# Kernel tuning notes

Hardware: AMD Instinct MI355X
Metric: run time of the kernel (lower is better)

## Reference

```python
import jax, jax.numpy as jnp
import numpy as np

V, E, H, L = 512, 128, 256, 4
B, T = 128, 1024


def setup_inputs() -> dict:
    key = jax.random.key(0)
    ks = jax.random.split(key, 16)
    s = 0.05
    inp = {
        "x": jax.random.randint(ks[0], (B, T), 0, V),
        "tags": jax.random.randint(ks[1], (B, T), 0, L),
        "mask": jnp.ones((B, T), dtype=bool),
        "emb": jax.random.normal(ks[2], (V, E), jnp.float32) * s,
        "w_ih_f": jax.random.normal(ks[3], (3 * H, E), jnp.float32) * s,
        "w_hh_f": jax.random.normal(ks[4], (3 * H, H), jnp.float32) * s,
        "b_ih_f": jax.random.normal(ks[5], (3 * H,), jnp.float32) * s,
        "b_hh_f": jax.random.normal(ks[6], (3 * H,), jnp.float32) * s,
        "w_ih_b": jax.random.normal(ks[7], (3 * H, E), jnp.float32) * s,
        "w_hh_b": jax.random.normal(ks[8], (3 * H, H), jnp.float32) * s,
        "b_ih_b": jax.random.normal(ks[9], (3 * H,), jnp.float32) * s,
        "b_hh_b": jax.random.normal(ks[10], (3 * H,), jnp.float32) * s,
        "fc_w": jax.random.normal(ks[11], (L, 2 * H), jnp.float32) * s,
        "fc_b": jax.random.normal(ks[12], (L,), jnp.float32) * s,
        "start_trans": jax.random.normal(ks[13], (L,), jnp.float32) * 0.1,
        "end_trans": jax.random.normal(ks[14], (L,), jnp.float32) * 0.1,
        "trans": jax.random.normal(ks[15], (L, L), jnp.float32) * 0.1,
    }
    return inp


def _gru_scan(xe, w_ih, w_hh, b_ih, b_hh):
    # xe: [B,T,E] -> out [B,T,H]; PyTorch GRU gate order: r, z, n
    gi = jnp.einsum("bte,ge->btg", xe, w_ih) + b_ih  # [B,T,3H]
    gi = jnp.swapaxes(gi, 0, 1)  # [T,B,3H]
    h0 = jnp.zeros((xe.shape[0], H), xe.dtype)

    def step(h, gi_t):
        gh = h @ w_hh.T + b_hh
        i_r, i_z, i_n = jnp.split(gi_t, 3, axis=-1)
        h_r, h_z, h_n = jnp.split(gh, 3, axis=-1)
        r = jax.nn.sigmoid(i_r + h_r)
        z = jax.nn.sigmoid(i_z + h_z)
        n = jnp.tanh(i_n + r * h_n)
        h_new = (1.0 - z) * n + z * h
        return h_new, h_new

    _, out = jax.lax.scan(step, h0, gi)
    return jnp.swapaxes(out, 0, 1)  # [B,T,H]


def _crf_neg_llh(emissions, tags, mask, start_trans, end_trans, trans):
    # emissions [B,T,L], tags [B,T] int, mask [B,T] bool
    maskf = mask.astype(emissions.dtype)
    # ----- numerator: score of gold path -----
    em_sel = jnp.take_along_axis(emissions, tags[..., None], axis=2)[..., 0]  # [B,T]
    trans_sel = trans[tags[:, :-1], tags[:, 1:]]  # [B,T-1]
    score = start_trans[tags[:, 0]] + em_sel[:, 0]
    score = score + jnp.sum((trans_sel + em_sel[:, 1:]) * maskf[:, 1:], axis=1)
    seq_ends = jnp.sum(mask.astype(jnp.int32), axis=1) - 1  # [B]
    last_tags = jnp.take_along_axis(tags, seq_ends[:, None], axis=1)[:, 0]
    score = score + end_trans[last_tags]
    # ----- denominator: forward algorithm (logsumexp scan) -----
    alpha0 = start_trans[None, :] + emissions[:, 0]  # [B,L]
    em_rest = jnp.swapaxes(emissions[:, 1:], 0, 1)  # [T-1,B,L]
    m_rest = jnp.swapaxes(mask[:, 1:], 0, 1)  # [T-1,B]

    def step(alpha, inputs):
        emit_t, m_t = inputs
        nxt = jax.nn.logsumexp(alpha[:, :, None] + trans[None] + emit_t[:, None, :], axis=1)
        alpha = jnp.where(m_t[:, None], nxt, alpha)
        return alpha, None

    alpha, _ = jax.lax.scan(step, alpha0, (em_rest, m_rest))
    logZ = jax.nn.logsumexp(alpha + end_trans[None, :], axis=1)  # [B]
    llh = score - logZ
    return -jnp.mean(llh)  # reduction='mean', negated in Segmenter.forward


def reference(x, tags, mask, emb, w_ih_f, w_hh_f, b_ih_f, b_hh_f,
              w_ih_b, w_hh_b, b_ih_b, b_hh_b, fc_w, fc_b,
              start_trans, end_trans, trans):
    xe = emb[x]  # [B,T,E]
    out_f = _gru_scan(xe, w_ih_f, w_hh_f, b_ih_f, b_hh_f)
    out_b = _gru_scan(xe[:, ::-1], w_ih_b, w_hh_b, b_ih_b, b_hh_b)[:, ::-1]
    gru_out = jnp.concatenate([out_f, out_b], axis=-1)  # [B,T,2H]
    emissions = jnp.einsum("bth,lh->btl", gru_out, fc_w) + fc_b  # [B,T,L]
    return _crf_neg_llh(emissions, tags, mask, start_trans, end_trans, trans)
```

## Files before the change

kernel.cpp:

```cpp
#include <hip/hip_runtime.h>
#include <hip/hip_fp16.h>

#define Tn 1024
#define NB 128

#define S_RZ (-1.4426950408889634f)
#define S_N  (-2.8853900817779268f)

typedef _Float16 h2_t  __attribute__((ext_vector_type(2)));
typedef _Float16 f16x8 __attribute__((ext_vector_type(8)));

__device__ __forceinline__ float dot2f(h2_t a, h2_t b, float c) {
#if __has_builtin(__builtin_amdgcn_fdot2)
  return __builtin_amdgcn_fdot2(a, b, c, false);
#else
  return c + (float)a[0] * (float)b[0] + (float)a[1] * (float)b[1];
#endif
}

__device__ __forceinline__ h2_t u2h(unsigned u) {
  union { unsigned u; h2_t h; } c; c.u = u; return c.h;
}

__global__ __launch_bounds__(768)
void gv_build(const float* __restrict__ emb,
              const float* __restrict__ wihf, const float* __restrict__ bihf, const float* __restrict__ bhhf,
              const float* __restrict__ wihb, const float* __restrict__ bihb, const float* __restrict__ bhhb,
              float* __restrict__ gv)
{
  const int d  = blockIdx.x >> 7;
  const int v4 = (blockIdx.x & 127) * 4;
  const float* wih = d ? wihb : wihf;
  const float* bih = d ? bihb : bihf;
  const float* bhh = d ? bhhb : bhhf;
  __shared__ float se[4][128];
  const int tid = threadIdx.x;
  if (tid < 512) se[tid >> 7][tid & 127] = emb[(v4 + (tid >> 7)) * 128 + (tid & 127)];
  __syncthreads();
  const int row = tid;
  const float b0 = bih[row];
  float a0 = b0, a1 = b0, a2 = b0, a3 = b0;
  #pragma unroll
  for (int e = 0; e < 128; e += 4) {
    const float4 w = *reinterpret_cast<const float4*>(&wih[row * 128 + e]);
    a0 = fmaf(w.x, se[0][e], a0); a0 = fmaf(w.y, se[0][e+1], a0);
    a0 = fmaf(w.z, se[0][e+2], a0); a0 = fmaf(w.w, se[0][e+3], a0);
    a1 = fmaf(w.x, se[1][e], a1); a1 = fmaf(w.y, se[1][e+1], a1);
    a1 = fmaf(w.z, se[1][e+2], a1); a1 = fmaf(w.w, se[1][e+3], a1);
    a2 = fmaf(w.x, se[2][e], a2); a2 = fmaf(w.y, se[2][e+1], a2);
    a2 = fmaf(w.z, se[2][e+2], a2); a2 = fmaf(w.w, se[2][e+3], a2);
    a3 = fmaf(w.x, se[3][e], a3); a3 = fmaf(w.y, se[3][e+1], a3);
    a3 = fmaf(w.z, se[3][e+2], a3); a3 = fmaf(w.w, se[3][e+3], a3);
  }
  const float sc  = (row < 512) ? S_RZ : S_N;
  const float add = (row < 512) ? bhh[row] : 0.f;
  float* out = gv + (size_t)(d * 512 + v4) * 768 + row;
  out[0]    = sc * (a0 + add);
  out[768]  = sc * (a1 + add);
  out[1536] = sc * (a2 + add);
  out[2304] = sc * (a3 + add);
}

#define DW(i) f16x8 WR##i, WZ##i, WN##i;
#define PKG(G, SC, i) { \
  const float4 _a = *reinterpret_cast<const float4*>(row##G + 8 * i); \
  const float4 _c = *reinterpret_cast<const float4*>(row##G + 8 * i + 4); \
  W##G##i[0] = (_Float16)(_a.x * (SC)); W##G##i[1] = (_Float16)(_a.y * (SC)); \
  W##G##i[2] = (_Float16)(_a.z * (SC)); W##G##i[3] = (_Float16)(_a.w * (SC)); \
  W##G##i[4] = (_Float16)(_c.x * (SC)); W##G##i[5] = (_Float16)(_c.y * (SC)); \
  W##G##i[6] = (_Float16)(_c.z * (SC)); W##G##i[7] = (_Float16)(_c.w * (SC)); }
#define PK3(i) PKG(R, S_RZ, i) PKG(Z, S_RZ, i) PKG(N, S_N, i)
#define SL(v, a, b) (__builtin_shufflevector(v, v, a, b))
#define DOT(i) { \
  const uint4 _hq = *reinterpret_cast<const uint4*>(hrow + 16 * i); \
  const h2_t _h0 = u2h(_hq.x), _h1 = u2h(_hq.y), _h2 = u2h(_hq.z), _h3 = u2h(_hq.w); \
  ar = dot2f(SL(WR##i,0,1), _h0, ar); az = dot2f(SL(WZ##i,0,1), _h0, az); an = dot2f(SL(WN##i,0,1), _h0, an); \
  ar = dot2f(SL(WR##i,2,3), _h1, ar); az = dot2f(SL(WZ##i,2,3), _h1, az); an = dot2f(SL(WN##i,2,3), _h1, an); \
  ar = dot2f(SL(WR##i,4,5), _h2, ar); az = dot2f(SL(WZ##i,4,5), _h2, az); an = dot2f(SL(WN##i,4,5), _h2, an); \
  ar = dot2f(SL(WR##i,6,7), _h3, ar); az = dot2f(SL(WZ##i,6,7), _h3, az); an = dot2f(SL(WN##i,6,7), _h3, an); }

__global__ __launch_bounds__(512, 2)
void gru_scan(const int* __restrict__ x,
              const float* __restrict__ gv,
              const float* __restrict__ whhf,
              const float* __restrict__ whhb,
              const float* __restrict__ bhhf,
              const float* __restrict__ bhhb,
              const float* __restrict__ fcw,
              float* __restrict__ em)
{
  const int tid  = threadIdx.x;
  const int j    = tid >> 1;
  const int half = tid & 1;
  const int dir  = blockIdx.x & 1;
  const int b    = blockIdx.x >> 1;

  const float* whh = dir ? whhb : whhf;
  const float* bhh = dir ? bhhb : bhhf;

  __shared__ __align__(16) char hls[2 * 544];
  __shared__ float els[2][8];

  if (tid < 68) reinterpret_cast<uint4*>(hls)[tid] = make_uint4(0, 0, 0, 0);

  DW(0) DW(1) DW(2) DW(3) DW(4) DW(5) DW(6) DW(7)
  DW(8) DW(9) DW(10) DW(11) DW(12) DW(13) DW(14) DW(15)
  {
    const float* rowR = whh + (size_t)j * 256 + half * 128;
    const float* rowZ = rowR + 256 * 256;
    const float* rowN = rowZ + 256 * 256;
    PK3(0) PK3(1) PK3(2) PK3(3)
    __builtin_amdgcn_sched_barrier(0);
    PK3(4) PK3(5) PK3(6) PK3(7)
    __builtin_amdgcn_sched_barrier(0);
    PK3(8) PK3(9) PK3(10) PK3(11)
    __builtin_amdgcn_sched_barrier(0);
    PK3(12) PK3(13) PK3(14) PK3(15)
    __builtin_amdgcn_sched_barrier(0);
  }

  const float bn2 = 0.5f * S_N * bhh[512 + j];

  const int w8 = tid >> 6;
  const int kh = w8 >> 2;
  const int p  = (tid & 63) >> 1;
  h2_t fe0, fe1;
  {
    const float4 f = *reinterpret_cast<const float4*>(
        fcw + (w8 & 3) * 512 + dir * 256 + kh * 128 + 4 * p);
    fe0[0] = (_Float16)f.x; fe0[1] = (_Float16)f.y;
    fe1[0] = (_Float16)f.z; fe1[1] = (_Float16)f.w;
  }
  const int kh_off = kh * 272 + 8 * p;
  const int hr_off = half * 272;
  const int hw_off = (j >> 7) * 272 + (j & 127) * 2;

  const float* gvd = gv + (size_t)dir * (512 * 768);
  const int*   xb  = x + b * Tn;
  float*       emo = em + (size_t)(dir * NB + b) * (Tn * 4);

  float ho = 0.f;
  int tok = xb[dir ? (Tn - 1) : 0];
  __syncthreads();

  for (int t = 0; t < Tn; ++t) {
    const int cur = t & 1;

    float gir = 0.f, giz = 0.f, gin = 0.f;
    if (!half) {
      const float* g = gvd + (size_t)tok * 768 + j;
      gir = g[0]; giz = g[256]; gin = g[512];
    }
    const int ntok = xb[dir ? (t + 2 <= Tn ? Tn - 2 - t : 0)
                           : (t + 1 < Tn ? t + 1 : 0)];

    if (t >= 2 && tid < 4) {
      const float v = els[cur ^ 1][tid] + els[cur ^ 1][tid + 4];
      const int ptt = dir ? (Tn - (t - 1)) : (t - 2);
      emo[ptt * 4 + tid] = v;
    }

    const char* hrow = hls + cur * 544 + hr_off;
    float ar = 0.f, az = 0.f, an = bn2;
    DOT(0) DOT(1) DOT(2) DOT(3)
    __builtin_amdgcn_sched_barrier(0);
    DOT(4) DOT(5) DOT(6) DOT(7)
    __builtin_amdgcn_sched_barrier(0);
    DOT(8) DOT(9) DOT(10) DOT(11)
    __builtin_amdgcn_sched_barrier(0);
    DOT(12) DOT(13) DOT(14) DOT(15)

    ar += __shfl_xor(ar, 1);
    az += __shfl_xor(az, 1);
    an += __shfl_xor(an, 1);

    if (!half) {
      const float er = __builtin_amdgcn_exp2f(gir + ar);
      const float r  = __builtin_amdgcn_rcpf(1.f + er);
      const float ez = __builtin_amdgcn_exp2f(giz + az);
      const float z  = __builtin_amdgcn_rcpf(1.f + ez);
      float y = fmaf(r, an, gin);
      y = fminf(y, 126.f);
      const float en = __builtin_amdgcn_exp2f(y);
      const float n  = (1.f - en) * __builtin_amdgcn_rcpf(1.f + en);
      const float hnew = fmaf(z, ho - n, n);
      ho = hnew;
      *reinterpret_cast<_Float16*>(hls + (cur ^ 1) * 544 + hw_off) = (_Float16)hnew;
    } else if (t > 0) {
      const uint2 hq = *reinterpret_cast<const uint2*>(hls + cur * 544 + kh_off);
      float pa = dot2f(fe0, u2h(hq.x), 0.f);
      pa = dot2f(fe1, u2h(hq.y), pa);
      pa += __shfl_xor(pa, 2);  pa += __shfl_xor(pa, 4);  pa += __shfl_xor(pa, 8);
      pa += __shfl_xor(pa, 16); pa += __shfl_xor(pa, 32);
      if ((tid & 63) == 1) els[t & 1][w8] = pa;
    }
    tok = ntok;
    __syncthreads();
  }

  if (tid < 4) {
    const float v = els[1][tid] + els[1][tid + 4];
    emo[(dir ? 1 : (Tn - 2)) * 4 + tid] = v;
  }
  if (half) {
    const uint2 hq = *reinterpret_cast<const uint2*>(hls + kh_off);
    float pa = dot2f(fe0, u2h(hq.x), 0.f);
    pa = dot2f(fe1, u2h(hq.y), pa);
    pa += __shfl_xor(pa, 2);  pa += __shfl_xor(pa, 4);  pa += __shfl_xor(pa, 8);
    pa += __shfl_xor(pa, 16); pa += __shfl_xor(pa, 32);
    if ((tid & 63) == 1) els[0][w8] = pa;
  }
  __syncthreads();
  if (tid < 4) {
    const float v = els[0][tid] + els[0][tid + 4];
    emo[(dir ? 0 : (Tn - 1)) * 4 + tid] = v;
  }
}

__global__ __launch_bounds__(64)
void crf_nllh(const int* __restrict__ tags,
              const float* __restrict__ em,
              const float* __restrict__ fc_b,
              const float* __restrict__ st,
              const float* __restrict__ et,
              const float* __restrict__ tr,
              float* __restrict__ llh)
{
  const int lane = threadIdx.x;
  const int l = lane & 3;
  const int q = lane >> 2;
  const int b = blockIdx.x * 16 + q;
  const float* ef = em + (size_t)b * Tn * 4;
  const float* eb = em + ((size_t)NB + b) * Tn * 4;
  const int* tg = tags + b * Tn;
  const float fcb = fc_b[l];
  const float tc0 = tr[l * 4 + l];
  const float tc1 = tr[(l ^ 1) * 4 + l];
  const float tc2 = tr[(l ^ 2) * 4 + l];
  const float tc3 = tr[(l ^ 3) * 4 + l];

  const float e0 = ef[l] + eb[l] + fcb;
  float alpha = st[l] + e0;
  int tprev = tg[0];
  float score = (tprev == l) ? (st[l] + e0) : 0.f;

  #pragma unroll 8
  for (int t = 1; t < Tn; ++t) {
    const float e = ef[t * 4 + l] + eb[t * 4 + l] + fcb;
    const int tc = tg[t];
    if (tc == l) {
      const int s2 = tprev ^ l;
      const float tsel = (s2 & 1) ? ((s2 & 2) ? tc3 : tc1)
                                  : ((s2 & 2) ? tc2 : tc0);
      score += e + tsel;
    }
    tprev = tc;
    const float a1 = __shfl_xor(alpha, 1);
    const float a2 = __shfl_xor(alpha, 2);
    const float a3 = __shfl_xor(alpha, 3);
    const float v0 = alpha + tc0;
    const float v1 = a1 + tc1;
    const float v2 = a2 + tc2;
    const float v3 = a3 + tc3;
    const float mx = fmaxf(fmaxf(v0, v1), fmaxf(v2, v3));
    const float s = __expf(v0 - mx) + __expf(v1 - mx) + __expf(v2 - mx) + __expf(v3 - mx);
    alpha = mx + __logf(s) + e;
  }

  score += (tprev == l) ? et[l] : 0.f;
  float ae = alpha + et[l];
  float m1 = fmaxf(ae, __shfl_xor(ae, 1));
  m1 = fmaxf(m1, __shfl_xor(m1, 2));
  float se = __expf(ae - m1);
  se += __shfl_xor(se, 1);
  se += __shfl_xor(se, 2);
  const float logZ = m1 + __logf(se);
  float sc = score + __shfl_xor(score, 1);
  sc += __shfl_xor(sc, 2);
  if (l == 0) llh[b] = sc - logZ;
}

__global__ __launch_bounds__(128)
void reduce_mean(const float* __restrict__ llh, float* __restrict__ out)
{
  const int t = threadIdx.x;
  float v = llh[t];
  #pragma unroll
  for (int m = 32; m >= 1; m >>= 1) v += __shfl_xor(v, m);
  __shared__ float s2[2];
  if ((t & 63) == 0) s2[t >> 6] = v;
  __syncthreads();
  if (t == 0) out[0] = -(s2[0] + s2[1]) * (1.f / 128.f);
}

extern "C" void kernel_launch(void* const* d_in, const int* in_sizes, int n_in,
                              void* d_out, int out_size, void* d_ws, size_t ws_size,
                              hipStream_t stream) {
  const int*   x    = (const int*)d_in[0];
  const int*   tags = (const int*)d_in[1];
  const float* emb  = (const float*)d_in[3];
  const float* wihf = (const float*)d_in[4];
  const float* whhf = (const float*)d_in[5];
  const float* bihf = (const float*)d_in[6];
  const float* bhhf = (const float*)d_in[7];
  const float* wihb = (const float*)d_in[8];
  const float* whhb = (const float*)d_in[9];
  const float* bihb = (const float*)d_in[10];
  const float* bhhb = (const float*)d_in[11];
  const float* fcw  = (const float*)d_in[12];
  const float* fcb  = (const float*)d_in[13];
  const float* st   = (const float*)d_in[14];
  const float* et   = (const float*)d_in[15];
  const float* tr   = (const float*)d_in[16];

  char* ws = (char*)d_ws;
  float* gv  = (float*)ws;
  float* em  = (float*)(ws + 3145728);
  float* llh = (float*)(ws + 3145728 + 4194304);

  gv_build<<<dim3(256), dim3(768), 0, stream>>>(emb, wihf, bihf, bhhf, wihb, bihb, bhhb, gv);
  gru_scan<<<dim3(256), dim3(512), 0, stream>>>(x, gv, whhf, whhb, bhhf, bhhb, fcw, em);
  crf_nllh<<<dim3(8), dim3(64), 0, stream>>>(tags, em, fcb, st, et, tr, llh);
  reduce_mean<<<dim3(1), dim3(128), 0, stream>>>(llh, (float*)d_out);
}
```

Measured before the change: 1.829 ms.

## Compute GRU recurrent matvec with MFMA and prefetch gate inputs via LDS

The per-step h·W_hh product, previously done with fdot2 split across thread pairs, now runs on MFMA 16x16x32 f16 instructions. The weights stay in registers as B fragments and h is broadcast as the A operand, so only one useful row of the output is used. gv_build writes the input-gate table in a permuted layout, and the next step's gate row is staged into a double-buffered LDS array so the global-load latency overlaps the current step. The emission projection is rebuilt with DPP reductions across all threads. This trades wasted MFMA rows and extra LDS traffic for a shorter serial dependency chain per timestep.

```diff
diff --git a/kernel.cpp b/kernel.cpp
--- a/kernel.cpp
+++ b/kernel.cpp
@@ -9,6 +9,7 @@
 
 typedef _Float16 h2_t  __attribute__((ext_vector_type(2)));
 typedef _Float16 f16x8 __attribute__((ext_vector_type(8)));
+typedef float    f32x4 __attribute__((ext_vector_type(4)));
 
 __device__ __forceinline__ float dot2f(h2_t a, h2_t b, float c) {
 #if __has_builtin(__builtin_amdgcn_fdot2)
@@ -22,11 +23,18 @@
   union { unsigned u; h2_t h; } c; c.u = u; return c.h;
 }
 
+template <int CTRL>
+__device__ __forceinline__ float dppadd(float v) {
+  int i = __builtin_bit_cast(int, v);
+  int r = __builtin_amdgcn_update_dpp(i, i, CTRL, 0xF, 0xF, true);
+  return v + __builtin_bit_cast(float, r);
+}
+
 __global__ __launch_bounds__(768)
 void gv_build(const float* __restrict__ emb,
               const float* __restrict__ wihf, const float* __restrict__ bihf, const float* __restrict__ bhhf,
               const float* __restrict__ wihb, const float* __restrict__ bihb, const float* __restrict__ bhhb,
-              float* __restrict__ gv)
+              float* __restrict__ gvp)
 {
   const int d  = blockIdx.x >> 7;
   const int v4 = (blockIdx.x & 127) * 4;
@@ -52,36 +60,21 @@
     a3 = fmaf(w.x, se[3][e], a3); a3 = fmaf(w.y, se[3][e+1], a3);
     a3 = fmaf(w.z, se[3][e+2], a3); a3 = fmaf(w.w, se[3][e+3], a3);
   }
-  const float sc  = (row < 512) ? S_RZ : S_N;
-  const float add = (row < 512) ? bhh[row] : 0.f;
-  float* out = gv + (size_t)(d * 512 + v4) * 768 + row;
+  const int g  = row >> 8, j = row & 255;
+  const int w  = j >> 5, tu = (j >> 4) & 1, c = j & 15;
+  const float sc  = (g == 2) ? S_N : S_RZ;
+  const float add = (g < 2) ? bhh[row] : 0.f;
+  const int slot = ((w * 2 + tu) * 3 + g) * 16 + c;
+  float* out = gvp + (size_t)(d * 512 + v4) * 768 + slot;
   out[0]    = sc * (a0 + add);
   out[768]  = sc * (a1 + add);
   out[1536] = sc * (a2 + add);
   out[2304] = sc * (a3 + add);
 }
 
-#define DW(i) f16x8 WR##i, WZ##i, WN##i;
-#define PKG(G, SC, i) { \
-  const float4 _a = *reinterpret_cast<const float4*>(row##G + 8 * i); \
-  const float4 _c = *reinterpret_cast<const float4*>(row##G + 8 * i + 4); \
-  W##G##i[0] = (_Float16)(_a.x * (SC)); W##G##i[1] = (_Float16)(_a.y * (SC)); \
-  W##G##i[2] = (_Float16)(_a.z * (SC)); W##G##i[3] = (_Float16)(_a.w * (SC)); \
-  W##G##i[4] = (_Float16)(_c.x * (SC)); W##G##i[5] = (_Float16)(_c.y * (SC)); \
-  W##G##i[6] = (_Float16)(_c.z * (SC)); W##G##i[7] = (_Float16)(_c.w * (SC)); }
-#define PK3(i) PKG(R, S_RZ, i) PKG(Z, S_RZ, i) PKG(N, S_N, i)
-#define SL(v, a, b) (__builtin_shufflevector(v, v, a, b))
-#define DOT(i) { \
-  const uint4 _hq = *reinterpret_cast<const uint4*>(hrow + 16 * i); \
-  const h2_t _h0 = u2h(_hq.x), _h1 = u2h(_hq.y), _h2 = u2h(_hq.z), _h3 = u2h(_hq.w); \
-  ar = dot2f(SL(WR##i,0,1), _h0, ar); az = dot2f(SL(WZ##i,0,1), _h0, az); an = dot2f(SL(WN##i,0,1), _h0, an); \
-  ar = dot2f(SL(WR##i,2,3), _h1, ar); az = dot2f(SL(WZ##i,2,3), _h1, az); an = dot2f(SL(WN##i,2,3), _h1, an); \
-  ar = dot2f(SL(WR##i,4,5), _h2, ar); az = dot2f(SL(WZ##i,4,5), _h2, az); an = dot2f(SL(WN##i,4,5), _h2, an); \
-  ar = dot2f(SL(WR##i,6,7), _h3, ar); az = dot2f(SL(WZ##i,6,7), _h3, az); an = dot2f(SL(WN##i,6,7), _h3, an); }
-
 __global__ __launch_bounds__(512, 2)
 void gru_scan(const int* __restrict__ x,
-              const float* __restrict__ gv,
+              const float* __restrict__ gvp,
               const float* __restrict__ whhf,
               const float* __restrict__ whhb,
               const float* __restrict__ bhhf,
@@ -89,130 +82,174 @@
               const float* __restrict__ fcw,
               float* __restrict__ em)
 {
-  const int tid  = threadIdx.x;
-  const int j    = tid >> 1;
-  const int half = tid & 1;
-  const int dir  = blockIdx.x & 1;
-  const int b    = blockIdx.x >> 1;
+  const int tid = threadIdx.x;
+  const int w   = tid >> 6;
+  const int l   = tid & 63;
+  const int c   = l & 15;
+  const int lg  = l >> 4;
+  const int dir = blockIdx.x & 1;
+  const int b   = blockIdx.x >> 1;
 
   const float* whh = dir ? whhb : whhf;
   const float* bhh = dir ? bhhb : bhhf;
 
-  __shared__ __align__(16) char hls[2 * 544];
+  __shared__ __align__(16) _Float16 hls[2][256];
+  __shared__ float gvs[2][768];
   __shared__ float els[2][8];
 
-  if (tid < 68) reinterpret_cast<uint4*>(hls)[tid] = make_uint4(0, 0, 0, 0);
-
-  DW(0) DW(1) DW(2) DW(3) DW(4) DW(5) DW(6) DW(7)
-  DW(8) DW(9) DW(10) DW(11) DW(12) DW(13) DW(14) DW(15)
-  {
-    const float* rowR = whh + (size_t)j * 256 + half * 128;
-    const float* rowZ = rowR + 256 * 256;
-    const float* rowN = rowZ + 256 * 256;
-    PK3(0) PK3(1) PK3(2) PK3(3)
-    __builtin_amdgcn_sched_barrier(0);
-    PK3(4) PK3(5) PK3(6) PK3(7)
-    __builtin_amdgcn_sched_barrier(0);
-    PK3(8) PK3(9) PK3(10) PK3(11)
-    __builtin_amdgcn_sched_barrier(0);
-    PK3(12) PK3(13) PK3(14) PK3(15)
-    __builtin_amdgcn_sched_barrier(0);
-  }
-
-  const float bn2 = 0.5f * S_N * bhh[512 + j];
-
-  const int w8 = tid >> 6;
-  const int kh = w8 >> 2;
-  const int p  = (tid & 63) >> 1;
-  h2_t fe0, fe1;
-  {
-    const float4 f = *reinterpret_cast<const float4*>(
-        fcw + (w8 & 3) * 512 + dir * 256 + kh * 128 + 4 * p);
-    fe0[0] = (_Float16)f.x; fe0[1] = (_Float16)f.y;
-    fe1[0] = (_Float16)f.z; fe1[1] = (_Float16)f.w;
-  }
-  const int kh_off = kh * 272 + 8 * p;
-  const int hr_off = half * 272;
-  const int hw_off = (j >> 7) * 272 + (j & 127) * 2;
-
-  const float* gvd = gv + (size_t)dir * (512 * 768);
+  if (tid < 64) reinterpret_cast<uint4*>(hls)[tid] = make_uint4(0, 0, 0, 0);
+
+  f16x8 bf[3][2][8];
+  #pragma unroll
+  for (int g = 0; g < 3; ++g) {
+    const float sc = (g == 2) ? S_N : S_RZ;
+    #pragma unroll
+    for (int tu = 0; tu < 2; ++tu) {
+      const float* wrow = whh + (size_t)(g * 256 + w * 32 + tu * 16 + c) * 256 + lg * 8;
+      #pragma unroll
+      for (int ks = 0; ks < 8; ++ks) {
+        const float4 f0 = *reinterpret_cast<const float4*>(wrow + ks * 32);
+        const float4 f1 = *reinterpret_cast<const float4*>(wrow + ks * 32 + 4);
+        f16x8 v;
+        v[0] = (_Float16)(f0.x * sc); v[1] = (_Float16)(f0.y * sc);
+        v[2] = (_Float16)(f0.z * sc); v[3] = (_Float16)(f0.w * sc);
+        v[4] = (_Float16)(f1.x * sc); v[5] = (_Float16)(f1.y * sc);
+        v[6] = (_Float16)(f1.z * sc); v[7] = (_Float16)(f1.w * sc);
+        bf[g][tu][ks] = v;
+      }
+    }
+  }
+
+  const float bn0 = S_N * bhh[512 + w * 32 + c];
+  const float bn1 = S_N * bhh[512 + w * 32 + 16 + c];
+
+  const int lab = tid >> 7;
+  const int kp  = tid & 127;
+  h2_t fce;
+  fce[0] = (_Float16)fcw[lab * 512 + dir * 256 + 2 * kp];
+  fce[1] = (_Float16)fcw[lab * 512 + dir * 256 + 2 * kp + 1];
+
   const int*   xb  = x + b * Tn;
   float*       emo = em + (size_t)(dir * NB + b) * (Tn * 4);
-
-  float ho = 0.f;
-  int tok = xb[dir ? (Tn - 1) : 0];
+  const float* gvd = gvp + (size_t)dir * (512 * 768);
+
+  {
+    const float* gr = gvd + (size_t)xb[dir ? (Tn - 1) : 0] * 768;
+    gvs[0][tid] = gr[tid];
+    if (tid < 256) gvs[0][tid + 512] = gr[tid + 512];
+  }
+  float ho0 = 0.f, ho1 = 0.f;
   __syncthreads();
 
   for (int t = 0; t < Tn; ++t) {
     const int cur = t & 1;
 
-    float gir = 0.f, giz = 0.f, gin = 0.f;
-    if (!half) {
-      const float* g = gvd + (size_t)tok * 768 + j;
-      gir = g[0]; giz = g[256]; gin = g[512];
-    }
-    const int ntok = xb[dir ? (t + 2 <= Tn ? Tn - 2 - t : 0)
-                           : (t + 1 < Tn ? t + 1 : 0)];
-
+    const int tn1 = (t + 1 < Tn) ? (t + 1) : (Tn - 1);
+    const float* gr = gvd + (size_t)xb[dir ? (Tn - 1 - tn1) : tn1] * 768;
+    const float su0 = gr[tid];
+    const float su1 = (tid < 256) ? gr[tid + 512] : 0.f;
+
+    {
+      const unsigned hq = *reinterpret_cast<const unsigned*>(&hls[cur][kp * 2]);
+      float pa = dot2f(fce, u2h(hq), 0.f);
+      pa = dppadd<0xB1>(pa);
+      pa = dppadd<0x4E>(pa);
+      pa = dppadd<0x141>(pa);
+      pa = dppadd<0x140>(pa);
+      pa += __shfl_xor(pa, 16);
+      pa += __shfl_xor(pa, 32);
+      if (l == 0) els[cur][w] = pa;
+    }
     if (t >= 2 && tid < 4) {
-      const float v = els[cur ^ 1][tid] + els[cur ^ 1][tid + 4];
-      const int ptt = dir ? (Tn - (t - 1)) : (t - 2);
+      const float v = els[cur ^ 1][2 * tid] + els[cur ^ 1][2 * tid + 1];
+      const int ptt = dir ? (Tn + 1 - t) : (t - 2);
       emo[ptt * 4 + tid] = v;
     }
 
-    const char* hrow = hls + cur * 544 + hr_off;
-    float ar = 0.f, az = 0.f, an = bn2;
-    DOT(0) DOT(1) DOT(2) DOT(3)
+    const float* gc = gvs[cur] + w * 96 + c;
+    f32x4 aR0 = {gc[0],  0.f, 0.f, 0.f};
+    f32x4 aZ0 = {gc[16], 0.f, 0.f, 0.f};
+    f32x4 aN0 = {bn0,    0.f, 0.f, 0.f};
+    f32x4 aR1 = {gc[48], 0.f, 0.f, 0.f};
+    f32x4 aZ1 = {gc[64], 0.f, 0.f, 0.f};
+    f32x4 aN1 = {bn1,    0.f, 0.f, 0.f};
+    const float gin0 = gc[32];
+    const float gin1 = gc[80];
+
+    const _Float16* hc = hls[cur];
+    #pragma unroll
+    for (int ks = 0; ks < 4; ++ks) {
+      const f16x8 a = *reinterpret_cast<const f16x8*>(hc + ks * 32 + lg * 8);
+      aR0 = __builtin_amdgcn_mfma_f32_16x16x32_f16(a, bf[0][0][ks], aR0, 0, 0, 0);
+      aZ0 = __builtin_amdgcn_mfma_f32_16x16x32_f16(a, bf[1][0][ks], aZ0, 0, 0, 0);
+      aN0 = __builtin_amdgcn_mfma_f32_16x16x32_f16(a, bf[2][0][ks], aN0, 0, 0, 0);
+      aR1 = __builtin_amdgcn_mfma_f32_16x16x32_f16(a, bf[0][1][ks], aR1, 0, 0, 0);
+      aZ1 = __builtin_amdgcn_mfma_f32_16x16x32_f16(a, bf[1][1][ks], aZ1, 0, 0, 0);
+      aN1 = __builtin_amdgcn_mfma_f32_16x16x32_f16(a, bf[2][1][ks], aN1, 0, 0, 0);
+    }
     __builtin_amdgcn_sched_barrier(0);
-    DOT(4) DOT(5) DOT(6) DOT(7)
-    __builtin_amdgcn_sched_barrier(0);
-    DOT(8) DOT(9) DOT(10) DOT(11)
-    __builtin_amdgcn_sched_barrier(0);
-    DOT(12) DOT(13) DOT(14) DOT(15)
-
-    ar += __shfl_xor(ar, 1);
-    az += __shfl_xor(az, 1);
-    an += __shfl_xor(an, 1);
-
-    if (!half) {
-      const float er = __builtin_amdgcn_exp2f(gir + ar);
-      const float r  = __builtin_amdgcn_rcpf(1.f + er);
-      const float ez = __builtin_amdgcn_exp2f(giz + az);
-      const float z  = __builtin_amdgcn_rcpf(1.f + ez);
-      float y = fmaf(r, an, gin);
-      y = fminf(y, 126.f);
-      const float en = __builtin_amdgcn_exp2f(y);
-      const float n  = (1.f - en) * __builtin_amdgcn_rcpf(1.f + en);
-      const float hnew = fmaf(z, ho - n, n);
-      ho = hnew;
-      *reinterpret_cast<_Float16*>(hls + (cur ^ 1) * 544 + hw_off) = (_Float16)hnew;
-    } else if (t > 0) {
-      const uint2 hq = *reinterpret_cast<const uint2*>(hls + cur * 544 + kh_off);
-      float pa = dot2f(fe0, u2h(hq.x), 0.f);
-      pa = dot2f(fe1, u2h(hq.y), pa);
-      pa += __shfl_xor(pa, 2);  pa += __shfl_xor(pa, 4);  pa += __shfl_xor(pa, 8);
-      pa += __shfl_xor(pa, 16); pa += __shfl_xor(pa, 32);
-      if ((tid & 63) == 1) els[t & 1][w8] = pa;
-    }
-    tok = ntok;
+    #pragma unroll
+    for (int ks = 4; ks < 8; ++ks) {
+      const f16x8 a = *reinterpret_cast<const f16x8*>(hc + ks * 32 + lg * 8);
+      aR0 = __builtin_amdgcn_mfma_f32_16x16x32_f16(a, bf[0][0][ks], aR0, 0, 0, 0);
+      aZ0 = __builtin_amdgcn_mfma_f32_16x16x32_f16(a, bf[1][0][ks], aZ0, 0, 0, 0);
+      aN0 = __builtin_amdgcn_mfma_f32_16x16x32_f16(a, bf[2][0][ks], aN0, 0, 0, 0);
+      aR1 = __builtin_amdgcn_mfma_f32_16x16x32_f16(a, bf[0][1][ks], aR1, 0, 0, 0);
+      aZ1 = __builtin_amdgcn_mfma_f32_16x16x32_f16(a, bf[1][1][ks], aZ1, 0, 0, 0);
+      aN1 = __builtin_amdgcn_mfma_f32_16x16x32_f16(a, bf[2][1][ks], aN1, 0, 0, 0);
+    }
+
+    {
+      const float er0 = __builtin_amdgcn_exp2f(aR0[0]);
+      const float rr0 = __builtin_amdgcn_rcpf(1.f + er0);
+      const float ez0 = __builtin_amdgcn_exp2f(aZ0[0]);
+      const float zz0 = __builtin_amdgcn_rcpf(1.f + ez0);
+      float y0 = fmaf(rr0, aN0[0], gin0);
+      y0 = fminf(y0, 126.f);
+      const float en0 = __builtin_amdgcn_exp2f(y0);
+      const float nn0 = (1.f - en0) * __builtin_amdgcn_rcpf(1.f + en0);
+      const float h0 = fmaf(zz0, ho0 - nn0, nn0);
+
+      const float er1 = __builtin_amdgcn_exp2f(aR1[0]);
+      const float rr1 = __builtin_amdgcn_rcpf(1.f + er1);
+      const float ez1 = __builtin_amdgcn_exp2f(aZ1[0]);
+      const float zz1 = __builtin_amdgcn_rcpf(1.f + ez1);
+      float y1 = fmaf(rr1, aN1[0], gin1);
+      y1 = fminf(y1, 126.f);
+      const float en1 = __builtin_amdgcn_exp2f(y1);
+      const float nn1 = (1.f - en1) * __builtin_amdgcn_rcpf(1.f + en1);
+      const float h1 = fmaf(zz1, ho1 - nn1, nn1);
+
+      ho0 = h0; ho1 = h1;
+      if (lg == 0) {
+        hls[cur ^ 1][w * 32 + c]      = (_Float16)h0;
+        hls[cur ^ 1][w * 32 + 16 + c] = (_Float16)h1;
+      }
+    }
+
+    gvs[cur ^ 1][tid] = su0;
+    if (tid < 256) gvs[cur ^ 1][tid + 512] = su1;
     __syncthreads();
   }
 
   if (tid < 4) {
-    const float v = els[1][tid] + els[1][tid + 4];
+    const float v = els[1][2 * tid] + els[1][2 * tid + 1];
     emo[(dir ? 1 : (Tn - 2)) * 4 + tid] = v;
   }
-  if (half) {
-    const uint2 hq = *reinterpret_cast<const uint2*>(hls + kh_off);
-    float pa = dot2f(fe0, u2h(hq.x), 0.f);
-    pa = dot2f(fe1, u2h(hq.y), pa);
-    pa += __shfl_xor(pa, 2);  pa += __shfl_xor(pa, 4);  pa += __shfl_xor(pa, 8);
-    pa += __shfl_xor(pa, 16); pa += __shfl_xor(pa, 32);
-    if ((tid & 63) == 1) els[0][w8] = pa;
+  {
+    const unsigned hq = *reinterpret_cast<const unsigned*>(&hls[0][kp * 2]);
+    float pa = dot2f(fce, u2h(hq), 0.f);
+    pa = dppadd<0xB1>(pa);
+    pa = dppadd<0x4E>(pa);
+    pa = dppadd<0x141>(pa);
+    pa = dppadd<0x140>(pa);
+    pa += __shfl_xor(pa, 16);
+    pa += __shfl_xor(pa, 32);
+    if (l == 0) els[0][w] = pa;
   }
   __syncthreads();
   if (tid < 4) {
-    const float v = els[0][tid] + els[0][tid + 4];
+    const float v = els[0][2 * tid] + els[0][2 * tid + 1];
     emo[(dir ? 0 : (Tn - 1)) * 4 + tid] = v;
   }
 }
@@ -314,12 +351,12 @@
   const float* tr   = (const float*)d_in[16];
 
   char* ws = (char*)d_ws;
-  float* gv  = (float*)ws;
+  float* gvp = (float*)ws;
   float* em  = (float*)(ws + 3145728);
   float* llh = (float*)(ws + 3145728 + 4194304);
 
-  gv_build<<<dim3(256), dim3(768), 0, stream>>>(emb, wihf, bihf, bhhf, wihb, bihb, bhhb, gv);
-  gru_scan<<<dim3(256), dim3(512), 0, stream>>>(x, gv, whhf, whhb, bhhf, bhhb, fcw, em);
+  gv_build<<<dim3(256), dim3(768), 0, stream>>>(emb, wihf, bihf, bhhf, wihb, bihb, bhhb, gvp);
+  gru_scan<<<dim3(256), dim3(512), 0, stream>>>(x, gvp, whhf, whhb, bhhf, bhhb, fcw, em);
   crf_nllh<<<dim3(8), dim3(64), 0, stream>>>(tags, em, fcb, st, et, tr, llh);
   reduce_mean<<<dim3(1), dim3(128), 0, stream>>>(llh, (float*)d_out);
 }
```

Result: faster. 1.759 ms (-3.8%).
